# Performance work log

Hardware: AMD Instinct MI355X
Metric: run time of the kernel (lower is better)

Reference implementation:

```python
import jax, jax.numpy as jnp
import numpy as np
import math

B, S, DIM, H = 2, 2048, 1024, 16
Q_DIM = 64                 # cfg.pair_dim
V_DIM = Q_DIM * 3 // 2     # 96
MAX_POS = 2048             # cfg.rope_max_position
EPS = 1e-8
SOFTCAP = 5.0


def apply_rope(x):
    # x: [B, S, H, D]; faithful to torch version: freq = 1/logspace(0, log10(max_pos), D//2)
    D = x.shape[-1]
    nf = D // 2
    freq = 1.0 / jnp.logspace(0.0, math.log10(MAX_POS), nf, dtype=x.dtype)   # [nf]
    positions = jnp.arange(x.shape[1], dtype=x.dtype)                         # [S]
    theta = positions[:, None] * freq                                         # [S, nf]
    sin_t = jnp.sin(theta)[None, :, None, :]                                  # [1,S,1,nf]
    cos_t = jnp.cos(theta)[None, :, None, :]
    x1 = x[..., ::2]
    x2 = x[..., 1::2]
    return jnp.concatenate([x1 * cos_t - x2 * sin_t, x1 * sin_t + x2 * cos_t], axis=-1)


def setup_inputs() -> dict:
    key = jax.random.key(0)
    ks = jax.random.split(key, 9)
    x = jax.random.normal(ks[0], (B, S, DIM), dtype=jnp.float32)
    attention_bias = jax.random.normal(ks[1], (B, H, S, S), dtype=jnp.float32)
    rms_weight = jnp.ones((DIM,), dtype=jnp.float32)
    sd = 1.0 / math.sqrt(DIM)
    Wq = jax.random.normal(ks[2], (DIM, H * Q_DIM), dtype=jnp.float32) * sd
    Wk = jax.random.normal(ks[3], (DIM, Q_DIM), dtype=jnp.float32) * sd
    Wv = jax.random.normal(ks[4], (DIM, V_DIM), dtype=jnp.float32) * sd
    bv = jax.random.normal(ks[5], (V_DIM,), dtype=jnp.float32) * sd
    Wo = jax.random.normal(ks[6], (H * V_DIM, DIM), dtype=jnp.float32) / math.sqrt(H * V_DIM)
    bo = jax.random.normal(ks[7], (DIM,), dtype=jnp.float32) * sd
    return {"x": x, "attention_bias": attention_bias, "rms_weight": rms_weight,
            "Wq": Wq, "Wk": Wk, "Wv": Wv, "bv": bv, "Wo": Wo, "bo": bo}


def reference(x, attention_bias, rms_weight, Wq, Wk, Wv, bv, Wo, bo):
    # RMSNorm
    xn = x * rms_weight / jnp.sqrt(jnp.mean(x * x, axis=-1, keepdims=True) + EPS)
    # projections (MQA: single shared k and v head)
    q = (xn @ Wq).reshape(B, S, H, Q_DIM)          # [B,S,H,Dq]
    k = xn @ Wk                                     # [B,S,Dq]
    v = xn @ Wv + bv                                # [B,S,Dv]
    # RoPE
    q = apply_rope(q)
    k = apply_rope(k[:, :, None, :])[:, :, 0, :]
    # attention logits with tanh soft-cap and external bias: [B,H,S,S]
    logits = jnp.einsum('bihd,bjd->bhij', q, k)
    logits = jnp.tanh((logits + attention_bias) / SOFTCAP) * SOFTCAP
    attn = jax.nn.softmax(logits, axis=-1)
    # context: shared V across heads
    ctx = jnp.einsum('bhij,bjd->bihd', attn, v).reshape(B, S, H * V_DIM)
    return ctx @ Wo + bo
```

## Files before the change

### kernel.cpp

```cpp
#include <hip/hip_runtime.h>
#include <math.h>

#define B_   2
#define S_   2048
#define DIM_ 1024
#define H_   16
#define QD_  64
#define VD_  96
#define NQKV 1184
#define EPS_ 1e-8f

using half_t = _Float16;
using half8  = __attribute__((ext_vector_type(8))) _Float16;
using half4v = __attribute__((ext_vector_type(4))) _Float16;
using f32x4  = __attribute__((ext_vector_type(4))) float;

__global__ __launch_bounds__(256) void rmsnorm_h(const float* __restrict__ x,
                                                 const float* __restrict__ w,
                                                 half_t* __restrict__ xn) {
    int row = blockIdx.x;
    int t = threadIdx.x;
    float4 v = ((const float4*)(x + (size_t)row * DIM_))[t];
    float ss = v.x * v.x + v.y * v.y + v.z * v.z + v.w * v.w;
#pragma unroll
    for (int off = 32; off > 0; off >>= 1) ss += __shfl_down(ss, off, 64);
    __shared__ float wsum[4];
    if ((t & 63) == 0) wsum[t >> 6] = ss;
    __syncthreads();
    float tot = wsum[0] + wsum[1] + wsum[2] + wsum[3];
    float scale = rsqrtf(tot * (1.0f / DIM_) + EPS_);
    float4 wv = ((const float4*)w)[t];
    half4v o;
    o[0] = (half_t)(v.x * wv.x * scale);
    o[1] = (half_t)(v.y * wv.y * scale);
    o[2] = (half_t)(v.z * wv.z * scale);
    o[3] = (half_t)(v.w * wv.w * scale);
    ((half4v*)(xn + (size_t)row * DIM_))[t] = o;
}

template <typename TIN>
__global__ __launch_bounds__(256) void transpose_cvt(const TIN* __restrict__ in,
                                                     half_t* __restrict__ out,
                                                     int R, int C, int ldin,
                                                     size_t zin, size_t zout) {
    __shared__ float tile[32][33];
    in += (size_t)blockIdx.z * zin;
    out += (size_t)blockIdx.z * zout;
    int tx = threadIdx.x & 31, ty = threadIdx.x >> 5;
#pragma unroll
    for (int i = 0; i < 32; i += 8) {
        int r = blockIdx.y * 32 + ty + i, c = blockIdx.x * 32 + tx;
        tile[ty + i][tx] = (float)in[(size_t)r * ldin + c];
    }
    __syncthreads();
#pragma unroll
    for (int i = 0; i < 32; i += 8) {
        int orow = blockIdx.x * 32 + ty + i, ocol = blockIdx.y * 32 + tx;
        out[(size_t)orow * R + ocol] = (half_t)tile[tx][ty + i];
    }
}

__global__ __launch_bounds__(256) void fill_qkv_bias(const float* __restrict__ bv,
                                                     float* __restrict__ bq) {
    int i = blockIdx.x * 256 + threadIdx.x;
    if (i < NQKV) bq[i] = (i >= H_ * QD_ + QD_) ? bv[i - (H_ * QD_ + QD_)] : 0.0f;
}

template <typename OutT, bool BIAS>
__global__ __launch_bounds__(256) void gemm_h(const half_t* __restrict__ A,
                                              const half_t* __restrict__ BT,
                                              OutT* __restrict__ C,
                                              const float* __restrict__ bias,
                                              int M, int N, int K) {
    __shared__ half_t As[128][40];
    __shared__ half_t Bs[128][40];
    int t = threadIdx.x;
    int w = t >> 6, lane = t & 63, l15 = lane & 15, l4 = lane >> 4;
    int wm = (w >> 1) * 64, wn = (w & 1) * 64;
    int m0 = blockIdx.y * 128, n0 = blockIdx.x * 128;
    int r0 = t >> 2, off0 = (t & 3) * 8;
    f32x4 acc[4][4] = {};
    const half8 hz = {};

    const half_t* Ap0 = A + (size_t)(m0 + r0) * K + off0;
    const half_t* Ap1 = Ap0 + (size_t)64 * K;
    const half_t* Bp0 = BT + (size_t)(n0 + r0) * K + off0;
    const half_t* Bp1 = Bp0 + (size_t)64 * K;
    bool bok0 = (n0 + r0) < N, bok1 = (n0 + r0 + 64) < N;

    half8 a0 = *(const half8*)Ap0;
    half8 a1 = *(const half8*)Ap1;
    half8 b0 = bok0 ? *(const half8*)Bp0 : hz;
    half8 b1 = bok1 ? *(const half8*)Bp1 : hz;

    for (int k0 = 0; k0 < K; k0 += 32) {
        __syncthreads();
        *(half8*)&As[r0][off0] = a0;
        *(half8*)&As[r0 + 64][off0] = a1;
        *(half8*)&Bs[r0][off0] = b0;
        *(half8*)&Bs[r0 + 64][off0] = b1;
        __syncthreads();
        if (k0 + 32 < K) {
            a0 = *(const half8*)(Ap0 + k0 + 32);
            a1 = *(const half8*)(Ap1 + k0 + 32);
            b0 = bok0 ? *(const half8*)(Bp0 + k0 + 32) : hz;
            b1 = bok1 ? *(const half8*)(Bp1 + k0 + 32) : hz;
        }
        half8 af[4], bf[4];
#pragma unroll
        for (int mt = 0; mt < 4; ++mt) af[mt] = *(const half8*)&As[wm + mt * 16 + l15][l4 * 8];
#pragma unroll
        for (int nt = 0; nt < 4; ++nt) bf[nt] = *(const half8*)&Bs[wn + nt * 16 + l15][l4 * 8];
#pragma unroll
        for (int mt = 0; mt < 4; ++mt)
#pragma unroll
            for (int nt = 0; nt < 4; ++nt)
                acc[mt][nt] =
                    __builtin_amdgcn_mfma_f32_16x16x32_f16(af[mt], bf[nt], acc[mt][nt], 0, 0, 0);
    }

#pragma unroll
    for (int mt = 0; mt < 4; ++mt)
#pragma unroll
        for (int nt = 0; nt < 4; ++nt) {
            int n = n0 + wn + nt * 16 + l15;
            if (n < N) {
#pragma unroll
                for (int reg = 0; reg < 4; ++reg) {
                    int m = m0 + wm + mt * 16 + l4 * 4 + reg;
                    float v = acc[mt][nt][reg];
                    if (BIAS) v += bias[n];
                    C[(size_t)m * N + n] = (OutT)v;
                }
            }
        }
}

__global__ __launch_bounds__(256) void rope_h(const half_t* __restrict__ in, int ldin,
                                              half_t* __restrict__ out,
                                              int hc, int total_pairs) {
    int p = blockIdx.x * 256 + threadIdx.x;
    if (p >= total_pairs) return;
    int i = p & 31;
    int chunk = p >> 5;
    int row = chunk / hc;
    int h = chunk - row * hc;
    int s = row & (S_ - 1);
    const half_t* src = in + (size_t)row * ldin + h * 64 + 2 * i;
    float x1 = (float)src[0], x2 = (float)src[1];
    float freq = exp2f((float)i * (-11.0f / 31.0f));
    float th = (float)s * freq;
    float sn, cs;
    sincosf(th, &sn, &cs);
    half_t* dst = out + (size_t)chunk * 64;
    dst[i] = (half_t)(x1 * cs - x2 * sn);
    dst[i + 32] = (half_t)(x1 * sn + x2 * cs);
}

__global__ __launch_bounds__(256, 4) void attn_mfma(const half_t* __restrict__ qh,
                                                    const half_t* __restrict__ kh,
                                                    const half_t* __restrict__ vt,
                                                    const float* __restrict__ bias,
                                                    half_t* __restrict__ ctx) {
    __shared__ half_t ks[64][72];
    __shared__ half_t vs[96][72];
    __shared__ float ps[4][16][68];

    int t = threadIdx.x;
    int w = t >> 6, lane = t & 63, l15 = lane & 15, l4 = lane >> 4;
    int i0 = blockIdx.x * 64, h = blockIdx.y, b = blockIdx.z;

    const half_t* qbase =
        qh + (((size_t)(b * S_ + i0 + w * 16 + l15) * H_ + h) << 6) + l4 * 8;
    half8 qf0 = *(const half8*)qbase;
    half8 qf1 = *(const half8*)(qbase + 32);

    f32x4 cacc[6] = {};
    float rsum[4] = {0.f, 0.f, 0.f, 0.f};

    int sr = t >> 3, so = (t & 7) * 8;
    const float* bbase =
        bias + ((size_t)(b * H_ + h) * S_ + i0 + w * 16 + l4 * 4) * S_ + l15;
    const half_t* krow0 = kh + (((size_t)b * S_ + sr) << 6) + so;
    const half_t* krow1 = krow0 + ((size_t)32 << 6);
    const half_t* vrow0 = vt + ((size_t)b * 96 + sr) * S_ + so;
    const half_t* vrow1 = vrow0 + (size_t)32 * S_;
    const half_t* vrow2 = vrow0 + (size_t)64 * S_;

    half8 kr0, kr1, vr0, vr1, vr2;
    float bc[16], bn[16];

    kr0 = *(const half8*)krow0;
    kr1 = *(const half8*)krow1;
    vr0 = *(const half8*)vrow0;
    vr1 = *(const half8*)vrow1;
    vr2 = *(const half8*)vrow2;
#pragma unroll
    for (int nt = 0; nt < 4; ++nt)
#pragma unroll
        for (int reg = 0; reg < 4; ++reg)
            bc[nt * 4 + reg] = bbase[nt * 16 + (size_t)reg * S_];

    *(half8*)&ks[sr][so] = kr0;
    *(half8*)&ks[sr + 32][so] = kr1;
    *(half8*)&vs[sr][so] = vr0;
    *(half8*)&vs[sr + 32][so] = vr1;
    *(half8*)&vs[sr + 64][so] = vr2;
    __syncthreads();

    for (int j0 = 0; j0 < S_; j0 += 64) {
        int jn = j0 + 64;
        bool more = jn < S_;

        if (more) {
            kr0 = *(const half8*)(krow0 + ((size_t)jn << 6));
            kr1 = *(const half8*)(krow1 + ((size_t)jn << 6));
            vr0 = *(const half8*)(vrow0 + jn);
            vr1 = *(const half8*)(vrow1 + jn);
            vr2 = *(const half8*)(vrow2 + jn);
#pragma unroll
            for (int nt = 0; nt < 4; ++nt)
#pragma unroll
                for (int reg = 0; reg < 4; ++reg)
                    bn[nt * 4 + reg] = bbase[jn + nt * 16 + (size_t)reg * S_];
        }

#pragma unroll
        for (int nt = 0; nt < 4; ++nt) {
            f32x4 s = {};
            half8 kb0 = *(const half8*)&ks[nt * 16 + l15][l4 * 8];
            half8 kb1 = *(const half8*)&ks[nt * 16 + l15][32 + l4 * 8];
            __builtin_amdgcn_s_setprio(1);
            s = __builtin_amdgcn_mfma_f32_16x16x32_f16(qf0, kb0, s, 0, 0, 0);
            s = __builtin_amdgcn_mfma_f32_16x16x32_f16(qf1, kb1, s, 0, 0, 0);
            __builtin_amdgcn_s_setprio(0);
#pragma unroll
            for (int reg = 0; reg < 4; ++reg) {
                float l = s[reg] + bc[nt * 4 + reg];
                float e2 = __expf(0.4f * l);
                float tnh = 1.0f - 2.0f * __builtin_amdgcn_rcpf(e2 + 1.0f);
                float p = __expf(5.0f * tnh);
                rsum[reg] += p;
                ps[w][l4 * 4 + reg][nt * 16 + l15] = p;
            }
        }

        half8 af[2];
#pragma unroll
        for (int kf = 0; kf < 2; ++kf) {
            f32x4 p0 = *(const f32x4*)&ps[w][l15][kf * 32 + l4 * 8];
            f32x4 p1 = *(const f32x4*)&ps[w][l15][kf * 32 + l4 * 8 + 4];
            half8 a;
#pragma unroll
            for (int e = 0; e < 4; ++e) {
                a[e] = (half_t)p0[e];
                a[e + 4] = (half_t)p1[e];
            }
            af[kf] = a;
        }
        __builtin_amdgcn_s_setprio(1);
#pragma unroll
        for (int nt = 0; nt < 6; ++nt) {
            half8 v0 = *(const half8*)&vs[nt * 16 + l15][l4 * 8];
            half8 v1 = *(const half8*)&vs[nt * 16 + l15][32 + l4 * 8];
            cacc[nt] = __builtin_amdgcn_mfma_f32_16x16x32_f16(af[0], v0, cacc[nt], 0, 0, 0);
            cacc[nt] = __builtin_amdgcn_mfma_f32_16x16x32_f16(af[1], v1, cacc[nt], 0, 0, 0);
        }
        __builtin_amdgcn_s_setprio(0);

        if (more) {
            __syncthreads();
            *(half8*)&ks[sr][so] = kr0;
            *(half8*)&ks[sr + 32][so] = kr1;
            *(half8*)&vs[sr][so] = vr0;
            *(half8*)&vs[sr + 32][so] = vr1;
            *(half8*)&vs[sr + 64][so] = vr2;
            __syncthreads();
#pragma unroll
            for (int q = 0; q < 16; ++q) bc[q] = bn[q];
        }
    }

#pragma unroll
    for (int m = 1; m < 16; m <<= 1)
#pragma unroll
        for (int reg = 0; reg < 4; ++reg) rsum[reg] += __shfl_xor(rsum[reg], m, 64);
    float rinv[4];
#pragma unroll
    for (int reg = 0; reg < 4; ++reg) rinv[reg] = __builtin_amdgcn_rcpf(rsum[reg]);

#pragma unroll
    for (int nt = 0; nt < 6; ++nt)
#pragma unroll
        for (int reg = 0; reg < 4; ++reg) {
            int i = i0 + w * 16 + l4 * 4 + reg;
            ctx[((size_t)(b * S_ + i) * H_ + h) * VD_ + nt * 16 + l15] =
                (half_t)(cacc[nt][reg] * rinv[reg]);
        }
}

extern "C" void kernel_launch(void* const* d_in, const int* in_sizes, int n_in,
                              void* d_out, int out_size, void* d_ws, size_t ws_size,
                              hipStream_t stream) {
    (void)in_sizes; (void)n_in; (void)out_size; (void)ws_size;
    const float* x  = (const float*)d_in[0];
    const float* ab = (const float*)d_in[1];
    const float* rw = (const float*)d_in[2];
    const float* Wq = (const float*)d_in[3];
    const float* Wk = (const float*)d_in[4];
    const float* Wv = (const float*)d_in[5];
    const float* bv = (const float*)d_in[6];
    const float* Wo = (const float*)d_in[7];
    const float* bo = (const float*)d_in[8];
    float* out = (float*)d_out;

    const size_t R = (size_t)B_ * S_;
    half_t* p = (half_t*)d_ws;
    half_t* xn_h  = p;  p += R * DIM_;
    half_t* qkv_h = p;  p += R * NQKV;
    half_t* q_h   = p;  p += R * DIM_;
    half_t* k_h   = p;  p += R * QD_;
    half_t* vtb   = p;  p += R * VD_;
    half_t* ctx_h = p;  p += R * H_ * VD_;
    half_t* WqkvT = p;  p += (size_t)NQKV * DIM_;
    half_t* WoT   = p;  p += (size_t)(H_ * VD_) * DIM_;
    float*  bqkv  = (float*)p;  p += 2 * NQKV;

    rmsnorm_h<<<dim3(R), 256, 0, stream>>>(x, rw, xn_h);

    half_t* WqT = WqkvT;
    half_t* WkT = WqkvT + (size_t)(H_ * QD_) * DIM_;
    half_t* WvT = WkT + (size_t)QD_ * DIM_;
    transpose_cvt<float><<<dim3(32, 32, 1), 256, 0, stream>>>(Wq, WqT, DIM_, H_ * QD_,
                                                              H_ * QD_, 0, 0);
    transpose_cvt<float><<<dim3(2, 32, 1), 256, 0, stream>>>(Wk, WkT, DIM_, QD_, QD_, 0, 0);
    transpose_cvt<float><<<dim3(3, 32, 1), 256, 0, stream>>>(Wv, WvT, DIM_, VD_, VD_, 0, 0);
    transpose_cvt<float><<<dim3(32, 48, 1), 256, 0, stream>>>(Wo, WoT, H_ * VD_, DIM_,
                                                              DIM_, 0, 0);
    fill_qkv_bias<<<dim3((NQKV + 255) / 256), 256, 0, stream>>>(bv, bqkv);

    gemm_h<half_t, true><<<dim3(10, 32), 256, 0, stream>>>(xn_h, WqkvT, qkv_h, bqkv,
                                                           (int)R, NQKV, DIM_);

    rope_h<<<dim3((R * H_ * 32) / 256), 256, 0, stream>>>(qkv_h, NQKV, q_h, H_,
                                                          (int)(R * H_ * 32));
    rope_h<<<dim3((R * 32) / 256), 256, 0, stream>>>(qkv_h + H_ * QD_, NQKV, k_h, 1,
                                                     (int)(R * 32));

    transpose_cvt<half_t><<<dim3(3, 64, 2), 256, 0, stream>>>(
        qkv_h + H_ * QD_ + QD_, vtb, S_, VD_, NQKV, (size_t)S_ * NQKV, (size_t)VD_ * S_);

    attn_mfma<<<dim3(S_ / 64, H_, B_), 256, 0, stream>>>(q_h, k_h, vtb, ab, ctx_h);

    gemm_h<float, true><<<dim3(8, 32), 256, 0, stream>>>(ctx_h, WoT, out, bo,
                                                         (int)R, DIM_, H_ * VD_);
}
```

Before: 826.5 us.

## Transpose QK MFMA so bias loads vectorize and P staging uses fp16

```diff
diff --git a/kernel.cpp b/kernel.cpp
--- a/kernel.cpp
+++ b/kernel.cpp
@@ -164,7 +164,7 @@
                                                     half_t* __restrict__ ctx) {
     __shared__ half_t ks[64][72];
     __shared__ half_t vs[96][72];
-    __shared__ float ps[4][16][68];
+    __shared__ half_t ps[4][16][72];
 
     int t = threadIdx.x;
     int w = t >> 6, lane = t & 63, l15 = lane & 15, l4 = lane >> 4;
@@ -176,11 +176,11 @@
     half8 qf1 = *(const half8*)(qbase + 32);
 
     f32x4 cacc[6] = {};
-    float rsum[4] = {0.f, 0.f, 0.f, 0.f};
+    float rsum = 0.f;
 
     int sr = t >> 3, so = (t & 7) * 8;
     const float* bbase =
-        bias + ((size_t)(b * H_ + h) * S_ + i0 + w * 16 + l4 * 4) * S_ + l15;
+        bias + ((size_t)(b * H_ + h) * S_ + i0 + w * 16 + l15) * S_ + l4 * 4;
     const half_t* krow0 = kh + (((size_t)b * S_ + sr) << 6) + so;
     const half_t* krow1 = krow0 + ((size_t)32 << 6);
     const half_t* vrow0 = vt + ((size_t)b * 96 + sr) * S_ + so;
@@ -188,7 +188,7 @@
     const half_t* vrow2 = vrow0 + (size_t)64 * S_;
 
     half8 kr0, kr1, vr0, vr1, vr2;
-    float bc[16], bn[16];
+    f32x4 bc[4], bn[4];
 
     kr0 = *(const half8*)krow0;
     kr1 = *(const half8*)krow1;
@@ -196,10 +196,7 @@
     vr1 = *(const half8*)vrow1;
     vr2 = *(const half8*)vrow2;
 #pragma unroll
-    for (int nt = 0; nt < 4; ++nt)
-#pragma unroll
-        for (int reg = 0; reg < 4; ++reg)
-            bc[nt * 4 + reg] = bbase[nt * 16 + (size_t)reg * S_];
+    for (int nt = 0; nt < 4; ++nt) bc[nt] = *(const f32x4*)(bbase + nt * 16);
 
     *(half8*)&ks[sr][so] = kr0;
     *(half8*)&ks[sr + 32][so] = kr1;
@@ -219,54 +216,41 @@
             vr1 = *(const half8*)(vrow1 + jn);
             vr2 = *(const half8*)(vrow2 + jn);
 #pragma unroll
-            for (int nt = 0; nt < 4; ++nt)
-#pragma unroll
-                for (int reg = 0; reg < 4; ++reg)
-                    bn[nt * 4 + reg] = bbase[jn + nt * 16 + (size_t)reg * S_];
-        }
-
-#pragma unroll
-        for (int nt = 0; nt < 4; ++nt) {
-            f32x4 s = {};
-            half8 kb0 = *(const half8*)&ks[nt * 16 + l15][l4 * 8];
-            half8 kb1 = *(const half8*)&ks[nt * 16 + l15][32 + l4 * 8];
+            for (int nt = 0; nt < 4; ++nt) bn[nt] = *(const f32x4*)(bbase + jn + nt * 16);
+        }
+
+#pragma unroll
+        for (int hf = 0; hf < 2; ++hf) {
+#pragma unroll
+            for (int nt = hf * 2; nt < hf * 2 + 2; ++nt) {
+                f32x4 s = {};
+                half8 kb0 = *(const half8*)&ks[nt * 16 + l15][l4 * 8];
+                half8 kb1 = *(const half8*)&ks[nt * 16 + l15][32 + l4 * 8];
+                __builtin_amdgcn_s_setprio(1);
+                s = __builtin_amdgcn_mfma_f32_16x16x32_f16(kb0, qf0, s, 0, 0, 0);
+                s = __builtin_amdgcn_mfma_f32_16x16x32_f16(kb1, qf1, s, 0, 0, 0);
+                __builtin_amdgcn_s_setprio(0);
+                half4v ph;
+#pragma unroll
+                for (int reg = 0; reg < 4; ++reg) {
+                    float l = s[reg] + bc[nt][reg];
+                    float e2 = __expf(0.4f * l);
+                    float tnh = 1.0f - 2.0f * __builtin_amdgcn_rcpf(e2 + 1.0f);
+                    float p = __expf(5.0f * tnh);
+                    rsum += p;
+                    ph[reg] = (half_t)p;
+                }
+                *(half4v*)&ps[w][l15][nt * 16 + l4 * 4] = ph;
+            }
+            half8 af = *(const half8*)&ps[w][l15][hf * 32 + l4 * 8];
             __builtin_amdgcn_s_setprio(1);
-            s = __builtin_amdgcn_mfma_f32_16x16x32_f16(qf0, kb0, s, 0, 0, 0);
-            s = __builtin_amdgcn_mfma_f32_16x16x32_f16(qf1, kb1, s, 0, 0, 0);
+#pragma unroll
+            for (int nt = 0; nt < 6; ++nt) {
+                half8 vv = *(const half8*)&vs[nt * 16 + l15][hf * 32 + l4 * 8];
+                cacc[nt] = __builtin_amdgcn_mfma_f32_16x16x32_f16(af, vv, cacc[nt], 0, 0, 0);
+            }
             __builtin_amdgcn_s_setprio(0);
-#pragma unroll
-            for (int reg = 0; reg < 4; ++reg) {
-                float l = s[reg] + bc[nt * 4 + reg];
-                float e2 = __expf(0.4f * l);
-                float tnh = 1.0f - 2.0f * __builtin_amdgcn_rcpf(e2 + 1.0f);
-                float p = __expf(5.0f * tnh);
-                rsum[reg] += p;
-                ps[w][l4 * 4 + reg][nt * 16 + l15] = p;
-            }
-        }
-
-        half8 af[2];
-#pragma unroll
-        for (int kf = 0; kf < 2; ++kf) {
-            f32x4 p0 = *(const f32x4*)&ps[w][l15][kf * 32 + l4 * 8];
-            f32x4 p1 = *(const f32x4*)&ps[w][l15][kf * 32 + l4 * 8 + 4];
-            half8 a;
-#pragma unroll
-            for (int e = 0; e < 4; ++e) {
-                a[e] = (half_t)p0[e];
-                a[e + 4] = (half_t)p1[e];
-            }
-            af[kf] = a;
-        }
-        __builtin_amdgcn_s_setprio(1);
-#pragma unroll
-        for (int nt = 0; nt < 6; ++nt) {
-            half8 v0 = *(const half8*)&vs[nt * 16 + l15][l4 * 8];
-            half8 v1 = *(const half8*)&vs[nt * 16 + l15][32 + l4 * 8];
-            cacc[nt] = __builtin_amdgcn_mfma_f32_16x16x32_f16(af[0], v0, cacc[nt], 0, 0, 0);
-            cacc[nt] = __builtin_amdgcn_mfma_f32_16x16x32_f16(af[1], v1, cacc[nt], 0, 0, 0);
-        }
-        __builtin_amdgcn_s_setprio(0);
+        }
 
         if (more) {
             __syncthreads();
@@ -277,17 +261,16 @@
             *(half8*)&vs[sr + 64][so] = vr2;
             __syncthreads();
 #pragma unroll
-            for (int q = 0; q < 16; ++q) bc[q] = bn[q];
+            for (int nt = 0; nt < 4; ++nt) bc[nt] = bn[nt];
         }
     }
 
-#pragma unroll
-    for (int m = 1; m < 16; m <<= 1)
-#pragma unroll
-        for (int reg = 0; reg < 4; ++reg) rsum[reg] += __shfl_xor(rsum[reg], m, 64);
-    float rinv[4];
-#pragma unroll
-    for (int reg = 0; reg < 4; ++reg) rinv[reg] = __builtin_amdgcn_rcpf(rsum[reg]);
+    rsum += __shfl_xor(rsum, 16, 64);
+    rsum += __shfl_xor(rsum, 32, 64);
+    float rinv = __builtin_amdgcn_rcpf(rsum);
+    float rr[4];
+#pragma unroll
+    for (int reg = 0; reg < 4; ++reg) rr[reg] = __shfl(rinv, l4 * 4 + reg, 64);
 
 #pragma unroll
     for (int nt = 0; nt < 6; ++nt)
@@ -295,7 +278,7 @@
         for (int reg = 0; reg < 4; ++reg) {
             int i = i0 + w * 16 + l4 * 4 + reg;
             ctx[((size_t)(b * S_ + i) * H_ + h) * VD_ + nt * 16 + l15] =
-                (half_t)(cacc[nt][reg] * rinv[reg]);
+                (half_t)(cacc[nt][reg] * rr[reg]);
         }
 }
 
```

After: 842.2 us. No clear change (+1.9%).
